# Kernel tuning notes

Measured on AMD Instinct MI355X. Metric: run time of the kernel, lower is better.

Reference implementation:

```python
import jax, jax.numpy as jnp
import numpy as np

B, T, F, H = 512, 1024, 64, 64  # batch, seq_len, n_feats, hidden


def setup_inputs() -> dict:
    key = jax.random.key(0)
    ks = jax.random.split(key, 12)
    s = 1.0 / np.sqrt(H)  # torch LSTM init scale: U(-1/sqrt(H), 1/sqrt(H))
    u = lambda k, shape: jax.random.uniform(k, shape, jnp.float32, -s, s)
    return {
        "x": jax.random.normal(ks[0], (B, T, F), jnp.float32),
        "w_ih0": u(ks[1], (4 * H, F)),
        "w_hh0": u(ks[2], (4 * H, H)),
        "b_ih0": u(ks[3], (4 * H,)),
        "b_hh0": u(ks[4], (4 * H,)),
        "w_ih1": u(ks[5], (4 * H, H)),
        "w_hh1": u(ks[6], (4 * H, H)),
        "b_ih1": u(ks[7], (4 * H,)),
        "b_hh1": u(ks[8], (4 * H,)),
        "fc_w": u(ks[9], (1, H)),
        "fc_b": u(ks[10], (1,)),
    }


def _lstm_layer(x, w_ih, w_hh, b_ih, b_hh):
    """Single LSTM layer, torch gate order (i, f, g, o). x: [B, T, in] -> [B, T, H]."""
    bsz = x.shape[0]
    h_dim = w_hh.shape[1]
    # Precompute all input projections in one big GEMM: [B, T, 4H]
    pre = jnp.einsum("bti,gi->btg", x, w_ih) + b_ih + b_hh

    def step(carry, p_t):
        h, c = carry
        z = p_t + h @ w_hh.T  # [B, 4H]
        i, f, g, o = jnp.split(z, 4, axis=-1)
        c = jax.nn.sigmoid(f) * c + jax.nn.sigmoid(i) * jnp.tanh(g)
        h = jax.nn.sigmoid(o) * jnp.tanh(c)
        return (h, c), h

    h0 = jnp.zeros((bsz, h_dim), x.dtype)
    (_, _), hs = jax.lax.scan(step, (h0, h0), jnp.swapaxes(pre, 0, 1))  # hs: [T, B, H]
    return jnp.swapaxes(hs, 0, 1)


def reference(x, w_ih0, w_hh0, b_ih0, b_hh0, w_ih1, w_hh1, b_ih1, b_hh1, fc_w, fc_b):
    h1 = _lstm_layer(x, w_ih0, w_hh0, b_ih0, b_hh0)   # [B, T, H]
    # (inter-layer dropout p=0.2 is train-only in torch; eval-mode reference omits it)
    h2 = _lstm_layer(h1, w_ih1, w_hh1, b_ih1, b_hh1)  # [B, T, H]
    return h2[:, -1] @ fc_w.T + fc_b                  # [B, 1]
```

## Files before the change

### kernel.cpp

```cpp
#include <hip/hip_runtime.h>
#include <hip/hip_bf16.h>


typedef _Float16 f16x8 __attribute__((ext_vector_type(8)));
typedef float f32x4  __attribute__((ext_vector_type(4)));

#define MFMAH(A, B, C) __builtin_amdgcn_mfma_f32_16x16x32_f16(A, B, C, 0, 0, 0)

constexpr int T_LEN = 1024;
constexpr int H     = 64;
constexpr int NCH   = 2;
constexpr int NTHR  = 1024;
constexpr int NBLK  = 256;

constexpr int    XT_HALFS   = 2 * 4 * 2 * 8;
constexpr size_t XBLK_HALFS = (size_t)T_LEN * XT_HALFS;

__device__ __forceinline__ float sigm_f(float x) {
  return __builtin_amdgcn_rcpf(1.0f + __expf(-x));
}
__device__ __forceinline__ float tanh_f(float x) {
  return 1.0f - 2.0f * __builtin_amdgcn_rcpf(1.0f + __expf(2.0f * x));
}
__device__ __forceinline__ unsigned dpp_xor1_u32(unsigned v) {
  return (unsigned)__builtin_amdgcn_mov_dpp((int)v, 0xB1, 0xF, 0xF, true);
}
__device__ __forceinline__ void lds_barrier() {
  asm volatile("s_waitcnt lgkmcnt(0)" ::: "memory");
  __builtin_amdgcn_s_barrier();
  asm volatile("" ::: "memory");
}

__global__ __launch_bounds__(256, 4) void xconv(const float* __restrict__ x,
                                                _Float16* __restrict__ xf) {
  const int gid = blockIdx.x * 256 + threadIdx.x;
  const int lq    = gid & 3;
  const int t     = (gid >> 2) & (T_LEN - 1);
  const int chain = gid >> 12;
  const int ch  = chain & 1;
  const int blk = chain >> 1;
  const float* src = x + ((size_t)chain * T_LEN + t) * H + 8 * lq;
  float4 v0 = *reinterpret_cast<const float4*>(src);
  float4 v1 = *reinterpret_cast<const float4*>(src + 4);
  float4 v2 = *reinterpret_cast<const float4*>(src + 32);
  float4 v3 = *reinterpret_cast<const float4*>(src + 36);
  float a[8]  = {v0.x, v0.y, v0.z, v0.w, v1.x, v1.y, v1.z, v1.w};
  float c8[8] = {v2.x, v2.y, v2.z, v2.w, v3.x, v3.y, v3.z, v3.w};
  f16x8 p0, p1;
#pragma unroll
  for (int e = 0; e < 8; ++e) {
    p0[e] = (_Float16)a[e];
    p1[e] = (_Float16)c8[e];
  }
  _Float16* dst = xf + (size_t)blk * XBLK_HALFS + (size_t)t * XT_HALFS +
                  lq * 16 + ch * 8;
  *reinterpret_cast<f16x8*>(dst)      = p0;
  *reinterpret_cast<f16x8*>(dst + 64) = p1;
}

__global__ __launch_bounds__(NTHR) void lstm_fused(
    const _Float16* __restrict__ xf,
    const float* __restrict__ w_ih0, const float* __restrict__ w_hh0,
    const float* __restrict__ b_ih0, const float* __restrict__ b_hh0,
    const float* __restrict__ w_ih1, const float* __restrict__ w_hh1,
    const float* __restrict__ b_ih1, const float* __restrict__ b_hh1,
    const float* __restrict__ fc_w, const float* __restrict__ fc_b,
    float* __restrict__ out) {
  const int tid = threadIdx.x;
  const int wv  = tid >> 6;
  const int L   = wv >> 3;
  const int w8  = wv & 7;
  const int l   = tid & 63;
  const int col = l & 15;
  const int lq  = l >> 4;
  const int blk = blockIdx.x;

  __shared__ __align__(16) _Float16 hb[2][2][128];
  __shared__ __align__(16) float zp[2][2][260];
  __shared__ float bias_s[2][256];
  __shared__ float fcw_s[H];
  __shared__ float hfin[NCH][H];

  for (int i = tid; i < 2 * 2 * 128; i += NTHR) ((_Float16*)hb)[i] = (_Float16)0.f;
  if (tid < 256)       bias_s[0][tid] = b_ih0[tid] + b_hh0[tid];
  else if (tid < 512)  bias_s[1][tid - 256] = b_ih1[tid - 256] + b_hh1[tid - 256];
  if (tid < H) fcw_s[tid] = fc_w[tid];

  const float* wih = L ? w_ih1 : w_ih0;
  const float* whh = L ? w_hh1 : w_hh0;
  f16x8 w16[2][4];
#pragma unroll
  for (int rt = 0; rt < 2; ++rt) {
#pragma unroll
    for (int kt = 0; kt < 4; ++kt) {
      const int row = 32 * w8 + 16 * rt + col;
      const int k0  = 32 * kt + 8 * lq;
      const float* src = (k0 < 64) ? &wih[row * 64 + k0] : &whh[row * 64 + (k0 - 64)];
      float4 v0 = *reinterpret_cast<const float4*>(src);
      float4 v1 = *reinterpret_cast<const float4*>(src + 4);
      float vv[8] = {v0.x, v0.y, v0.z, v0.w, v1.x, v1.y, v1.z, v1.w};
      f16x8 h8;
#pragma unroll
      for (int e = 0; e < 8; ++e) h8[e] = (_Float16)vv[e];
      w16[rt][kt] = h8;
    }
  }

  const int rdoff = lq * 16 + (col & 1) * 8;
  const bool is_gate = (wv < 2) || (wv == 10) || (wv == 11);
  const int gch = wv & 1;
  const int gh  = l;
  const int waddr_h = ((gh >> 5) << 6) + (((gh >> 3) & 3) << 4) + (gch << 3) + (gh & 7);
  float cst = 0.0f;

  const _Float16* xfl = xf + (size_t)blk * XBLK_HALFS + rdoff;
  f16x8 xb0, xb1, xbn0, xbn1;
  if (L == 0) {
    xb0 = *reinterpret_cast<const f16x8*>(xfl);
    xb1 = *reinterpret_cast<const f16x8*>(xfl + 64);
  }

  const f32x4 zf4 = {0.f, 0.f, 0.f, 0.f};

#define GATES(Lidx, hv_)                                            \
  {                                                                 \
    const float* zrow = &zp[Lidx][gch][0];                          \
    float z0 = zrow[gh]       + bias_s[Lidx][gh];                   \
    float z1 = zrow[64 + gh]  + bias_s[Lidx][64 + gh];              \
    float z2 = zrow[128 + gh] + bias_s[Lidx][128 + gh];             \
    float z3 = zrow[192 + gh] + bias_s[Lidx][192 + gh];             \
    float ig = sigm_f(z0), fg = sigm_f(z1);                         \
    float gg = tanh_f(z2), og = sigm_f(z3);                         \
    cst = fg * cst + ig * gg;                                       \
    hv_ = og * tanh_f(cst);                                         \
  }

#define HSTORE(base_, hv_)                                          \
  {                                                                 \
    _Float16 hf = (_Float16)(hv_);                                  \
    unsigned me = (unsigned)__builtin_bit_cast(unsigned short, hf); \
    unsigned nb = dpp_xor1_u32(me);                                 \
    if ((l & 1) == 0)                                               \
      reinterpret_cast<unsigned*>(base_)[waddr_h >> 1] = me | (nb << 16); \
  }

  __syncthreads();

  for (int t = 0; t <= T_LEN + 1; ++t) {
    if (L == 0) {
      if (t + 1 < T_LEN) {
        const _Float16* p = xfl + (size_t)(t + 1) * XT_HALFS;
        xbn0 = *reinterpret_cast<const f16x8*>(p);
        xbn1 = *reinterpret_cast<const f16x8*>(p + 64);
      }
      if (t < T_LEN) {
        const _Float16* h0c = &hb[0][(t + 1) & 1][0];
        f16x8 B2 = *reinterpret_cast<const f16x8*>(h0c + rdoff);
        f16x8 B3 = *reinterpret_cast<const f16x8*>(h0c + 64 + rdoff);
        f32x4 a0 = zf4, a1 = zf4;
        a0 = MFMAH(w16[0][0], xb0, a0); a1 = MFMAH(w16[1][0], xb0, a1);
        a0 = MFMAH(w16[0][1], xb1, a0); a1 = MFMAH(w16[1][1], xb1, a1);
        a0 = MFMAH(w16[0][2], B2,  a0); a1 = MFMAH(w16[1][2], B2,  a1);
        a0 = MFMAH(w16[0][3], B3,  a0); a1 = MFMAH(w16[1][3], B3,  a1);
        if (col < NCH) {
          *reinterpret_cast<f32x4*>(&zp[0][col][32 * w8 + 4 * lq])      = a0;
          *reinterpret_cast<f32x4*>(&zp[0][col][32 * w8 + 16 + 4 * lq]) = a1;
        }
      }
    } else if (is_gate) {
      if (t >= 2) {
        float hv;
        GATES(1, hv)
        if (t == T_LEN + 1) {
          hfin[gch][gh] = hv;
        } else {
          HSTORE(&hb[1][t & 1][0], hv)
        }
      }
    }

    lds_barrier();

    if (L == 0) {
      if (is_gate && t < T_LEN) {
        float hv;
        GATES(0, hv)
        HSTORE(&hb[0][t & 1][0], hv)
      }
    } else {
      if (t >= 1 && t <= T_LEN) {
        const _Float16* h0c = &hb[0][(t + 1) & 1][0];
        const _Float16* h1c = &hb[1][t & 1][0];
        f16x8 B0 = *reinterpret_cast<const f16x8*>(h0c + rdoff);
        f16x8 B1 = *reinterpret_cast<const f16x8*>(h0c + 64 + rdoff);
        f16x8 B2 = *reinterpret_cast<const f16x8*>(h1c + rdoff);
        f16x8 B3 = *reinterpret_cast<const f16x8*>(h1c + 64 + rdoff);
        f32x4 a0 = zf4, a1 = zf4;
        a0 = MFMAH(w16[0][0], B0, a0); a1 = MFMAH(w16[1][0], B0, a1);
        a0 = MFMAH(w16[0][1], B1, a0); a1 = MFMAH(w16[1][1], B1, a1);
        a0 = MFMAH(w16[0][2], B2, a0); a1 = MFMAH(w16[1][2], B2, a1);
        a0 = MFMAH(w16[0][3], B3, a0); a1 = MFMAH(w16[1][3], B3, a1);
        if (col < NCH) {
          *reinterpret_cast<f32x4*>(&zp[1][col][32 * w8 + 4 * lq])      = a0;
          *reinterpret_cast<f32x4*>(&zp[1][col][32 * w8 + 16 + 4 * lq]) = a1;
        }
      }
    }

    lds_barrier();
    if (L == 0) { xb0 = xbn0; xb1 = xbn1; }
  }
#undef GATES
#undef HSTORE

  if (tid < NCH) {
    float acc = fc_b[0];
#pragma unroll
    for (int h = 0; h < H; ++h) acc += fcw_s[h] * hfin[tid][h];
    out[blk * NCH + tid] = acc;
  }
}

extern "C" void kernel_launch(void* const* d_in, const int* in_sizes, int n_in,
                              void* d_out, int out_size, void* d_ws, size_t ws_size,
                              hipStream_t stream) {
  const float* x     = (const float*)d_in[0];
  const float* w_ih0 = (const float*)d_in[1];
  const float* w_hh0 = (const float*)d_in[2];
  const float* b_ih0 = (const float*)d_in[3];
  const float* b_hh0 = (const float*)d_in[4];
  const float* w_ih1 = (const float*)d_in[5];
  const float* w_hh1 = (const float*)d_in[6];
  const float* b_ih1 = (const float*)d_in[7];
  const float* b_hh1 = (const float*)d_in[8];
  const float* fc_w  = (const float*)d_in[9];
  const float* fc_b  = (const float*)d_in[10];
  float* out = (float*)d_out;

  _Float16* xfrag = (_Float16*)d_ws;

  xconv<<<dim3(8192), dim3(256), 0, stream>>>(x, xfrag);
  lstm_fused<<<dim3(NBLK), dim3(NTHR), 0, stream>>>(
      xfrag, w_ih0, w_hh0, b_ih0, b_hh0, w_ih1, w_hh1, b_ih1, b_hh1,
      fc_w, fc_b, out);
}
```

Before: 788.0 us.

## Fuse x fp16 conversion into LSTM kernel with two-step register prefetch

Removes the separate xconv pre-pass kernel that converted x to fp16 fragments in workspace. The LSTM kernel now reads fp32 x directly, prefetches raw floats two timesteps ahead and converts them to fp16 in the layer-0 wave one step ahead. This saves a kernel launch and a full write-then-read pass over a 128MB-scale buffer. In exchange the per-step loads are larger, less contiguous fp32 reads inside the latency-bound recurrence, and registers rise by 16 floats per thread.

```diff
diff --git a/kernel.cpp b/kernel.cpp
--- a/kernel.cpp
+++ b/kernel.cpp
@@ -13,9 +13,6 @@
 constexpr int NTHR  = 1024;
 constexpr int NBLK  = 256;
 
-constexpr int    XT_HALFS   = 2 * 4 * 2 * 8;
-constexpr size_t XBLK_HALFS = (size_t)T_LEN * XT_HALFS;
-
 __device__ __forceinline__ float sigm_f(float x) {
   return __builtin_amdgcn_rcpf(1.0f + __expf(-x));
 }
@@ -30,36 +27,17 @@
   __builtin_amdgcn_s_barrier();
   asm volatile("" ::: "memory");
 }
-
-__global__ __launch_bounds__(256, 4) void xconv(const float* __restrict__ x,
-                                                _Float16* __restrict__ xf) {
-  const int gid = blockIdx.x * 256 + threadIdx.x;
-  const int lq    = gid & 3;
-  const int t     = (gid >> 2) & (T_LEN - 1);
-  const int chain = gid >> 12;
-  const int ch  = chain & 1;
-  const int blk = chain >> 1;
-  const float* src = x + ((size_t)chain * T_LEN + t) * H + 8 * lq;
-  float4 v0 = *reinterpret_cast<const float4*>(src);
-  float4 v1 = *reinterpret_cast<const float4*>(src + 4);
-  float4 v2 = *reinterpret_cast<const float4*>(src + 32);
-  float4 v3 = *reinterpret_cast<const float4*>(src + 36);
-  float a[8]  = {v0.x, v0.y, v0.z, v0.w, v1.x, v1.y, v1.z, v1.w};
-  float c8[8] = {v2.x, v2.y, v2.z, v2.w, v3.x, v3.y, v3.z, v3.w};
-  f16x8 p0, p1;
-#pragma unroll
-  for (int e = 0; e < 8; ++e) {
-    p0[e] = (_Float16)a[e];
-    p1[e] = (_Float16)c8[e];
-  }
-  _Float16* dst = xf + (size_t)blk * XBLK_HALFS + (size_t)t * XT_HALFS +
-                  lq * 16 + ch * 8;
-  *reinterpret_cast<f16x8*>(dst)      = p0;
-  *reinterpret_cast<f16x8*>(dst + 64) = p1;
+__device__ __forceinline__ f16x8 cvt8(float4 u, float4 v) {
+  f16x8 r;
+  r[0] = (_Float16)u.x; r[1] = (_Float16)u.y;
+  r[2] = (_Float16)u.z; r[3] = (_Float16)u.w;
+  r[4] = (_Float16)v.x; r[5] = (_Float16)v.y;
+  r[6] = (_Float16)v.z; r[7] = (_Float16)v.w;
+  return r;
 }
 
 __global__ __launch_bounds__(NTHR) void lstm_fused(
-    const _Float16* __restrict__ xf,
+    const float* __restrict__ xin,
     const float* __restrict__ w_ih0, const float* __restrict__ w_hh0,
     const float* __restrict__ b_ih0, const float* __restrict__ b_hh0,
     const float* __restrict__ w_ih1, const float* __restrict__ w_hh1,
@@ -113,11 +91,21 @@
   const int waddr_h = ((gh >> 5) << 6) + (((gh >> 3) & 3) << 4) + (gch << 3) + (gh & 7);
   float cst = 0.0f;
 
-  const _Float16* xfl = xf + (size_t)blk * XBLK_HALFS + rdoff;
+  const float* xp = xin + ((size_t)(blk * NCH + (col & 1)) * T_LEN) * H + 8 * lq;
   f16x8 xb0, xb1, xbn0, xbn1;
+  float4 xr0, xr1, xr2, xr3;
   if (L == 0) {
-    xb0 = *reinterpret_cast<const f16x8*>(xfl);
-    xb1 = *reinterpret_cast<const f16x8*>(xfl + 64);
+    float4 a0_ = *reinterpret_cast<const float4*>(xp);
+    float4 a1_ = *reinterpret_cast<const float4*>(xp + 4);
+    float4 a2_ = *reinterpret_cast<const float4*>(xp + 32);
+    float4 a3_ = *reinterpret_cast<const float4*>(xp + 36);
+    xb0 = cvt8(a0_, a1_);
+    xb1 = cvt8(a2_, a3_);
+    const float* p = xp + H;
+    xr0 = *reinterpret_cast<const float4*>(p);
+    xr1 = *reinterpret_cast<const float4*>(p + 4);
+    xr2 = *reinterpret_cast<const float4*>(p + 32);
+    xr3 = *reinterpret_cast<const float4*>(p + 36);
   }
 
   const f32x4 zf4 = {0.f, 0.f, 0.f, 0.f};
@@ -148,11 +136,6 @@
 
   for (int t = 0; t <= T_LEN + 1; ++t) {
     if (L == 0) {
-      if (t + 1 < T_LEN) {
-        const _Float16* p = xfl + (size_t)(t + 1) * XT_HALFS;
-        xbn0 = *reinterpret_cast<const f16x8*>(p);
-        xbn1 = *reinterpret_cast<const f16x8*>(p + 64);
-      }
       if (t < T_LEN) {
         const _Float16* h0c = &hb[0][(t + 1) & 1][0];
         f16x8 B2 = *reinterpret_cast<const f16x8*>(h0c + rdoff);
@@ -186,6 +169,17 @@
         float hv;
         GATES(0, hv)
         HSTORE(&hb[0][t & 1][0], hv)
+      }
+      if (t + 1 < T_LEN) {
+        xbn0 = cvt8(xr0, xr1);
+        xbn1 = cvt8(xr2, xr3);
+      }
+      if (t + 2 < T_LEN) {
+        const float* p = xp + (size_t)(t + 2) * H;
+        xr0 = *reinterpret_cast<const float4*>(p);
+        xr1 = *reinterpret_cast<const float4*>(p + 4);
+        xr2 = *reinterpret_cast<const float4*>(p + 32);
+        xr3 = *reinterpret_cast<const float4*>(p + 36);
       }
     } else {
       if (t >= 1 && t <= T_LEN) {
@@ -237,10 +231,7 @@
   const float* fc_b  = (const float*)d_in[10];
   float* out = (float*)d_out;
 
-  _Float16* xfrag = (_Float16*)d_ws;
-
-  xconv<<<dim3(8192), dim3(256), 0, stream>>>(x, xfrag);
   lstm_fused<<<dim3(NBLK), dim3(NTHR), 0, stream>>>(
-      xfrag, w_ih0, w_hh0, b_ih0, b_hh0, w_ih1, w_hh1, b_ih1, b_hh1,
+      x, w_ih0, w_hh0, b_ih0, b_hh0, w_ih1, w_hh1, b_ih1, b_hh1,
       fc_w, fc_b, out);
 }
```

Measured after the change: 829.6 us. +5.3%, slower.
